# Optimization experiments

Hardware: AMD Instinct MI355X
Metric: run time of the kernel (lower is better)

Reference implementation:

```python
import jax, jax.numpy as jnp
import numpy as np

D, K = 128, 32
B, H, W = 16, 64, 64


def setup_inputs() -> dict:
    key = jax.random.key(0)
    k1, k2, k3 = jax.random.split(key, 3)
    x = jax.random.normal(k1, (B, D, H, W), dtype=jnp.float32)
    std1 = 1.0 / (K * D) ** 0.5
    codewords = jax.random.uniform(k2, (K, D), minval=-std1, maxval=std1, dtype=jnp.float32)
    scale = jax.random.uniform(k3, (K,), minval=-1.0, maxval=0.0, dtype=jnp.float32)
    return {"x": x, "codewords": codewords, "scale": scale}


def reference(x, codewords, scale):
    b = x.shape[0]
    # (B, D, H, W) -> (B, N, D)
    X = x.reshape(b, D, -1).transpose(0, 2, 1)
    # scaled L2: SL[b,n,k] = scale[k] * ||X[b,n] - C[k]||^2, expanded to avoid (B,N,K,D)
    x2 = jnp.sum(X * X, axis=-1)                      # (B, N)
    c2 = jnp.sum(codewords * codewords, axis=-1)      # (K,)
    xc = jnp.einsum('bnd,kd->bnk', X, codewords)      # (B, N, K)
    SL = scale[None, None, :] * (x2[:, :, None] - 2.0 * xc + c2[None, None, :])
    A = jax.nn.softmax(SL, axis=2)                    # (B, N, K)
    # E[b,k,d] = sum_n A[b,n,k] * (X[b,n,d] - C[k,d])
    E = jnp.einsum('bnk,bnd->bkd', A, X) - jnp.sum(A, axis=1)[:, :, None] * codewords[None, :, :]
    return E
```

## Files before the change

kernel.cpp:

```cpp
#include <hip/hip_runtime.h>
#include <hip/hip_bf16.h>


#define D_   128
#define K_   32
#define NPB  64
#define NTOT 4096

typedef __attribute__((ext_vector_type(8))) short bf16x8;
typedef __attribute__((ext_vector_type(4))) float f32x4;
typedef __attribute__((ext_vector_type(4))) short short4v;

__device__ __forceinline__ short f2b(float f) {
  return (short)__builtin_bit_cast(unsigned short, __float2bfloat16(f));
}

__global__ __launch_bounds__(256, 2) void enc_kernel(
    const float* __restrict__ x,
    const float* __restrict__ cw,
    const float* __restrict__ scale,
    float* __restrict__ ws)
{
  __shared__ __align__(16) short sNb[NPB * D_];
  __shared__ __align__(16) short sDb[D_ * NPB];
  __shared__ __align__(16) short sAb[K_ * NPB];
  __shared__ __align__(16) float sX2w[NPB * 4];
  __shared__ float sasum[K_];

  const int t  = threadIdx.x;
  const int w  = t >> 6;
  const int l  = t & 63;
  const int lr = l & 15;
  const int lg = l >> 4;
  const int b  = blockIdx.x >> 5;
  const int nbase = (blockIdx.x & 31) * 128;

  const int n4s = t & 15;
  const int d0  = (t >> 4) * 8;
  const float* xb = x + (size_t)b * D_ * NTOT + nbase;

  bf16x8 bC[2][4];
  float c2p0 = 0.f, c2p1 = 0.f;
  #pragma unroll
  for (int kt = 0; kt < 2; ++kt) {
    const float* crow = cw + (lr + 16 * kt) * D_ + lg * 8;
    #pragma unroll
    for (int s = 0; s < 4; ++s) {
      float4 v0 = *reinterpret_cast<const float4*>(crow + 32 * s);
      float4 v1 = *reinterpret_cast<const float4*>(crow + 32 * s + 4);
      float vv[8] = {v0.x, v0.y, v0.z, v0.w, v1.x, v1.y, v1.z, v1.w};
      bf16x8 f;
      float cs = 0.f;
      #pragma unroll
      for (int j = 0; j < 8; ++j) { f[j] = f2b(vv[j]); cs = fmaf(vv[j], vv[j], cs); }
      bC[kt][s] = f;
      if (kt == 0) c2p0 += cs; else c2p1 += cs;
    }
  }
  c2p0 += __shfl_xor(c2p0, 16); c2p0 += __shfl_xor(c2p0, 32);
  c2p1 += __shfl_xor(c2p1, 16); c2p1 += __shfl_xor(c2p1, 32);
  const float sc0 = scale[lr];
  const float sc1 = scale[lr + 16];

  float4 xs[8];
  #pragma unroll
  for (int j = 0; j < 8; ++j)
    xs[j] = *reinterpret_cast<const float4*>(xb + (size_t)(d0 + j) * NTOT + n4s * 4);
  if (t < K_) sasum[t] = 0.0f;

  #define STAGE_TILE()                                                        \
  {                                                                           \
    short xb16[8][4];                                                         \
    _Pragma("unroll")                                                         \
    for (int j = 0; j < 8; ++j) {                                             \
      xb16[j][0] = f2b(xs[j].x); xb16[j][1] = f2b(xs[j].y);                   \
      xb16[j][2] = f2b(xs[j].z); xb16[j][3] = f2b(xs[j].w);                   \
    }                                                                         \
    float p2[4] = {0.f, 0.f, 0.f, 0.f};                                       \
    _Pragma("unroll")                                                         \
    for (int j = 0; j < 8; ++j) {                                             \
      p2[0] = fmaf(xs[j].x, xs[j].x, p2[0]);                                  \
      p2[1] = fmaf(xs[j].y, xs[j].y, p2[1]);                                  \
      p2[2] = fmaf(xs[j].z, xs[j].z, p2[2]);                                  \
      p2[3] = fmaf(xs[j].w, xs[j].w, p2[3]);                                  \
    }                                                                         \
    _Pragma("unroll")                                                         \
    for (int i = 0; i < 4; ++i) {                                             \
      p2[i] += __shfl_xor(p2[i], 16);                                         \
      p2[i] += __shfl_xor(p2[i], 32);                                         \
    }                                                                         \
    if (lg == 0) {                                                            \
      _Pragma("unroll")                                                       \
      for (int i = 0; i < 4; ++i) sX2w[(n4s * 4 + i) * 4 + w] = p2[i];        \
    }                                                                         \
    _Pragma("unroll")                                                         \
    for (int i = 0; i < 4; ++i) {                                             \
      int n = n4s * 4 + i;                                                    \
      bf16x8 pk;                                                              \
      _Pragma("unroll")                                                       \
      for (int j = 0; j < 8; ++j) pk[j] = xb16[j][i];                         \
      int phys = ((d0 >> 3) ^ (n & 15)) & 15;                                 \
      *reinterpret_cast<bf16x8*>(&sNb[n * D_ + phys * 8]) = pk;               \
    }                                                                         \
    _Pragma("unroll")                                                         \
    for (int j = 0; j < 8; ++j) {                                             \
      int d = d0 + j;                                                         \
      int phys = ((n4s >> 1) ^ (d & 7) ^ ((d >> 3) & 7)) & 7;                 \
      short4v pk4 = {xb16[j][0], xb16[j][1], xb16[j][2], xb16[j][3]};         \
      *reinterpret_cast<short4v*>(&sDb[d * NPB + phys * 8 + (n4s & 1) * 4]) = pk4; \
    }                                                                         \
  }

  STAGE_TILE();
  __syncthreads();

  const int m0 = w * 16;
  const int nrow = m0 + lr;
  f32x4 acc[2][2];
  float asvT[2][4];
  #pragma unroll
  for (int mt = 0; mt < 2; ++mt) {
    #pragma unroll
    for (int dti = 0; dti < 2; ++dti) acc[mt][dti] = (f32x4){0.f, 0.f, 0.f, 0.f};
    #pragma unroll
    for (int r = 0; r < 4; ++r) asvT[mt][r] = 0.f;
  }

  #pragma unroll
  for (int tile = 0; tile < 2; ++tile) {
    if (tile == 0) {
      #pragma unroll
      for (int j = 0; j < 8; ++j)
        xs[j] = *reinterpret_cast<const float4*>(
            xb + 64 + (size_t)(d0 + j) * NTOT + n4s * 4);
    }

    f32x4 p0 = {0.f, 0.f, 0.f, 0.f}, p1 = {0.f, 0.f, 0.f, 0.f};
    #pragma unroll
    for (int s = 0; s < 4; ++s) {
      int dblk = 4 * s + lg;
      bf16x8 af = *reinterpret_cast<const bf16x8*>(
          &sNb[nrow * D_ + ((dblk ^ lr) & 15) * 8]);
      p0 = __builtin_amdgcn_mfma_f32_16x16x32_bf16(af, bC[0][s], p0, 0, 0, 0);
      p1 = __builtin_amdgcn_mfma_f32_16x16x32_bf16(af, bC[1][s], p1, 0, 0, 0);
    }
    float x2r[4];
    #pragma unroll
    for (int r = 0; r < 4; ++r) {
      float4 v = *reinterpret_cast<const float4*>(&sX2w[(m0 + lg * 4 + r) * 4]);
      x2r[r] = (v.x + v.y) + (v.z + v.w);
    }

    float a0[4], a1[4], mr[4], sr[4];
    #pragma unroll
    for (int r = 0; r < 4; ++r) {
      float sl0 = sc0 * (x2r[r] - 2.f * p0[r] + c2p0);
      float sl1 = sc1 * (x2r[r] - 2.f * p1[r] + c2p1);
      a0[r] = sl0; a1[r] = sl1;
      mr[r] = fmaxf(sl0, sl1);
    }
    #pragma unroll
    for (int dlt = 1; dlt <= 8; dlt <<= 1)
      #pragma unroll
      for (int r = 0; r < 4; ++r) mr[r] = fmaxf(mr[r], __shfl_xor(mr[r], dlt));
    #pragma unroll
    for (int r = 0; r < 4; ++r) {
      a0[r] = __expf(a0[r] - mr[r]);
      a1[r] = __expf(a1[r] - mr[r]);
      sr[r] = a0[r] + a1[r];
    }
    #pragma unroll
    for (int dlt = 1; dlt <= 8; dlt <<= 1)
      #pragma unroll
      for (int r = 0; r < 4; ++r) sr[r] += __shfl_xor(sr[r], dlt);
    #pragma unroll
    for (int r = 0; r < 4; ++r) {
      float inv = 1.0f / sr[r];
      a0[r] *= inv; a1[r] *= inv;
    }

    float as0 = a0[0] + a0[1] + a0[2] + a0[3];
    float as1 = a1[0] + a1[1] + a1[2] + a1[3];
    as0 += __shfl_xor(as0, 16); as0 += __shfl_xor(as0, 32);
    as1 += __shfl_xor(as1, 16); as1 += __shfl_xor(as1, 32);
    if (lg == 0) {
      atomicAdd(&sasum[lr], as0);
      atomicAdd(&sasum[lr + 16], as1);
    }
    #pragma unroll
    for (int r = 0; r < 4; ++r) {
      int n = m0 + lg * 4 + r;
      sAb[lr * 64 + (n ^ ((lr & 7) << 3))] = f2b(a0[r]);
      sAb[(lr + 16) * 64 + (n ^ (((lr + 16) & 7) << 3))] = f2b(a1[r]);
    }
    __syncthreads();

    bf16x8 aA[2][2];
    #pragma unroll
    for (int mt = 0; mt < 2; ++mt) {
      int k = mt * 16 + lr;
      #pragma unroll
      for (int s = 0; s < 2; ++s) {
        int nb = 32 * s + lg * 8;
        aA[mt][s] = *reinterpret_cast<const bf16x8*>(
            &sAb[k * 64 + (nb ^ ((k & 7) << 3))]);
      }
    }
    #pragma unroll
    for (int mt = 0; mt < 2; ++mt)
      #pragma unroll
      for (int r = 0; r < 4; ++r) asvT[mt][r] += sasum[mt * 16 + lg * 4 + r];
    #pragma unroll
    for (int s = 0; s < 2; ++s) {
      #pragma unroll
      for (int dti = 0; dti < 2; ++dti) {
        int d = (2 * w + dti) * 16 + lr;
        int phys = (((4 * s + lg) ^ (d & 7) ^ ((d >> 3) & 7)) & 7);
        bf16x8 bf = *reinterpret_cast<const bf16x8*>(&sDb[d * NPB + phys * 8]);
        acc[0][dti] = __builtin_amdgcn_mfma_f32_16x16x32_bf16(aA[0][s], bf, acc[0][dti], 0, 0, 0);
        acc[1][dti] = __builtin_amdgcn_mfma_f32_16x16x32_bf16(aA[1][s], bf, acc[1][dti], 0, 0, 0);
      }
    }
    __syncthreads();

    if (tile == 0) {
      if (t < K_) sasum[t] = 0.0f;
      STAGE_TILE();
      __syncthreads();
    }
  }

  float* wp = ws + (size_t)blockIdx.x * (K_ * D_);
  #pragma unroll
  for (int mt = 0; mt < 2; ++mt)
    #pragma unroll
    for (int dti = 0; dti < 2; ++dti) {
      int d = (2 * w + dti) * 16 + lr;
      #pragma unroll
      for (int r = 0; r < 4; ++r) {
        int k = mt * 16 + lg * 4 + r;
        wp[k * D_ + d] = acc[mt][dti][r] - asvT[mt][r] * cw[k * D_ + d];
      }
    }
}

__global__ __launch_bounds__(256) void reduce_kernel(
    const float* __restrict__ ws, float* __restrict__ out)
{
  int g = blockIdx.x * 256 + threadIdx.x;
  int b = g >> 10;
  int q = g & 1023;
  const float4* base = reinterpret_cast<const float4*>(ws) + (size_t)b * 32 * 1024 + q;
  float4 s = {0.f, 0.f, 0.f, 0.f};
  #pragma unroll
  for (int t = 0; t < 32; ++t) {
    float4 v = base[(size_t)t * 1024];
    s.x += v.x; s.y += v.y; s.z += v.z; s.w += v.w;
  }
  reinterpret_cast<float4*>(out)[g] = s;
}

extern "C" void kernel_launch(void* const* d_in, const int* in_sizes, int n_in,
                              void* d_out, int out_size, void* d_ws, size_t ws_size,
                              hipStream_t stream) {
  const float* x  = (const float*)d_in[0];
  const float* cw = (const float*)d_in[1];
  const float* sc = (const float*)d_in[2];
  float* out = (float*)d_out;
  float* ws  = (float*)d_ws;
  const int B = in_sizes[0] / (D_ * NTOT);
  enc_kernel<<<dim3(B * 32), dim3(256), 0, stream>>>(x, cw, sc, ws);
  reduce_kernel<<<dim3(B * 4096 / 4 / 256), dim3(256), 0, stream>>>(ws, out);
}
```

Baseline: 85.07 us.

## Fuse partial-sum reduction into encoder kernel via last-block atomic counter

Adds a templated fused path where each block increments a per-batch atomic counter after writing its partial, and the last block for each batch sums the 32 partials and writes the output. This removes the separate reduce kernel launch, replacing it with a small memset. The cost is a serialized tail reduction done by one block per batch, plus threadfence overhead. The path runs only when the workspace is large enough to hold the counters.

```diff
diff --git a/kernel.cpp b/kernel.cpp
--- a/kernel.cpp
+++ b/kernel.cpp
@@ -6,6 +6,7 @@
 #define K_   32
 #define NPB  64
 #define NTOT 4096
+#define PART_BYTES (512 * K_ * D_ * 4)
 
 typedef __attribute__((ext_vector_type(8))) short bf16x8;
 typedef __attribute__((ext_vector_type(4))) float f32x4;
@@ -15,17 +16,21 @@
   return (short)__builtin_bit_cast(unsigned short, __float2bfloat16(f));
 }
 
+template <int FUSED>
 __global__ __launch_bounds__(256, 2) void enc_kernel(
     const float* __restrict__ x,
     const float* __restrict__ cw,
     const float* __restrict__ scale,
-    float* __restrict__ ws)
+    float* __restrict__ ws,
+    int* __restrict__ cnt,
+    float* __restrict__ out)
 {
   __shared__ __align__(16) short sNb[NPB * D_];
   __shared__ __align__(16) short sDb[D_ * NPB];
   __shared__ __align__(16) short sAb[K_ * NPB];
   __shared__ __align__(16) float sX2w[NPB * 4];
   __shared__ float sasum[K_];
+  __shared__ int sIsLast;
 
   const int t  = threadIdx.x;
   const int w  = t >> 6;
@@ -242,6 +247,29 @@
         wp[k * D_ + d] = acc[mt][dti][r] - asvT[mt][r] * cw[k * D_ + d];
       }
     }
+
+  if (!FUSED) return;
+
+  __threadfence();
+  __syncthreads();
+  if (t == 0) sIsLast = (atomicAdd(&cnt[b], 1) == 31);
+  __syncthreads();
+  if (!sIsLast) return;
+  __threadfence();
+
+  const float4* base = reinterpret_cast<const float4*>(ws) + (size_t)b * 32 * 1024;
+  float4* ob = reinterpret_cast<float4*>(out) + (size_t)b * 1024;
+  #pragma unroll
+  for (int qi = 0; qi < 4; ++qi) {
+    int q = qi * 256 + t;
+    float4 s = {0.f, 0.f, 0.f, 0.f};
+    #pragma unroll 8
+    for (int p = 0; p < 32; ++p) {
+      float4 v = base[(size_t)p * 1024 + q];
+      s.x += v.x; s.y += v.y; s.z += v.z; s.w += v.w;
+    }
+    ob[q] = s;
+  }
 }
 
 __global__ __launch_bounds__(256) void reduce_kernel(
@@ -269,6 +297,12 @@
   float* out = (float*)d_out;
   float* ws  = (float*)d_ws;
   const int B = in_sizes[0] / (D_ * NTOT);
-  enc_kernel<<<dim3(B * 32), dim3(256), 0, stream>>>(x, cw, sc, ws);
-  reduce_kernel<<<dim3(B * 4096 / 4 / 256), dim3(256), 0, stream>>>(ws, out);
+  if (ws_size >= PART_BYTES + 256) {
+    int* cnt = (int*)((char*)d_ws + PART_BYTES);
+    hipMemsetAsync(cnt, 0, 64, stream);
+    enc_kernel<1><<<dim3(B * 32), dim3(256), 0, stream>>>(x, cw, sc, ws, cnt, out);
+  } else {
+    enc_kernel<0><<<dim3(B * 32), dim3(256), 0, stream>>>(x, cw, sc, ws, nullptr, out);
+    reduce_kernel<<<dim3(B * 4096 / 4 / 256), dim3(256), 0, stream>>>(ws, out);
+  }
 }
```

New measurement: 150.0 us. 76.3% more time.
